# Kernel optimization log

Measured on AMD Instinct MI355X. Metric: run time of the kernel, lower is better.

The kernel has to match this reference:

```python
import jax, jax.numpy as jnp
import numpy as np

DIM = 384
HEADS = 8
ADLA = 343
HWD = 14
N = HWD ** 3
B = 8
HEAD_DIM = DIM // HEADS
SCALE = HEAD_DIM ** -0.5
POOL = 7  # ceil(343**(1/3)); 14 is evenly divisible by 7


def _lin_mat(in_size, out_size):
    # PyTorch trilinear interpolation (align_corners=False), one axis -> (out,in) matrix
    scale = in_size / out_size
    x = (np.arange(out_size) + 0.5) * scale - 0.5
    x = np.clip(x, 0.0, in_size - 1)
    x0 = np.floor(x).astype(np.int64)
    x1 = np.minimum(x0 + 1, in_size - 1)
    w = (x - x0).astype(np.float32)
    M = np.zeros((out_size, in_size), np.float32)
    M[np.arange(out_size), x0] += 1.0 - w
    M[np.arange(out_size), x1] += w
    return jnp.asarray(M)


def _interp3(t, out_hwd):
    # t: (..., a, b, c) -> (..., H, W, D) trilinear, align_corners=False
    Ma = _lin_mat(t.shape[-3], out_hwd[0])
    Mb = _lin_mat(t.shape[-2], out_hwd[1])
    Mc = _lin_mat(t.shape[-1], out_hwd[2])
    return jnp.einsum('...abc,xa,yb,zc->...xyz', t, Ma, Mb, Mc)


def setup_inputs() -> dict:
    key = jax.random.key(0)
    ks = jax.random.split(key, 16)
    std = 0.02
    return {
        'x': jax.random.normal(ks[0], (B, N, DIM), jnp.float32),
        'Wq': jax.random.normal(ks[1], (DIM, DIM), jnp.float32) * std,
        'Wkv': jax.random.normal(ks[2], (DIM, 2 * DIM), jnp.float32) * std,
        'Wproj': jax.random.normal(ks[3], (DIM, DIM), jnp.float32) * std,
        'bproj': jnp.zeros((DIM,), jnp.float32),
        'dwc_w': jax.random.normal(ks[4], (DIM, 1, 3, 3, 3), jnp.float32) * std,
        'dwc_b': jnp.zeros((DIM,), jnp.float32),
        'an_bias': jax.random.normal(ks[5], (HEADS, ADLA, 7, 7, 7), jnp.float32) * std,
        'na_bias': jax.random.normal(ks[6], (HEADS, ADLA, 7, 7, 7), jnp.float32) * std,
        'ah_bias': jax.random.normal(ks[7], (1, HEADS, ADLA, HWD, 1, 1), jnp.float32) * std,
        'aw_bias': jax.random.normal(ks[8], (1, HEADS, ADLA, 1, HWD, 1), jnp.float32) * std,
        'ad_bias': jax.random.normal(ks[9], (1, HEADS, ADLA, 1, 1, HWD), jnp.float32) * std,
        'ha_bias': jax.random.normal(ks[10], (1, HEADS, HWD, 1, 1, ADLA), jnp.float32) * std,
        'wa_bias': jax.random.normal(ks[11], (1, HEADS, 1, HWD, 1, ADLA), jnp.float32) * std,
        'da_bias': jax.random.normal(ks[12], (1, HEADS, 1, 1, HWD, ADLA), jnp.float32) * std,
        'H': HWD, 'W': HWD, 'D': HWD,
    }


def reference(x, Wq, Wkv, Wproj, bproj, dwc_w, dwc_b, an_bias, na_bias,
              ah_bias, aw_bias, ad_bias, ha_bias, wa_bias, da_bias, H, W, D):
    b, n, c = x.shape
    h, hd = HEADS, c // HEADS
    q = x @ Wq                       # (b, n, c)
    kv = x @ Wkv                     # (b, n, 2c)  (sr_ratio == 1)
    k, v = kv[..., :c], kv[..., c:]
    # AdaptiveAvgPool3d 14->7: even 2x2x2 block mean; spatial flatten order matches torch
    adla = q.reshape(b, POOL, H // POOL, POOL, W // POOL, POOL, D // POOL, c)
    adla = adla.mean(axis=(2, 4, 6)).reshape(b, ADLA, c)   # (b, A, c)
    qh = q.reshape(b, n, h, hd).transpose(0, 2, 1, 3)       # (b,h,n,hd)
    kh = k.reshape(b, n, h, hd).transpose(0, 2, 1, 3)
    vh = v.reshape(b, n, h, hd).transpose(0, 2, 1, 3)
    ath = adla.reshape(b, ADLA, h, hd).transpose(0, 2, 1, 3)  # (b,h,A,hd)
    # stage 1: anchor -> tokens
    pb1 = _interp3(an_bias, (H, W, D)).reshape(1, h, ADLA, n)
    pb2 = (ah_bias + aw_bias + ad_bias).reshape(1, h, ADLA, n)
    logits1 = jnp.einsum('bhad,bhnd->bhan', ath * SCALE, kh) + pb1 + pb2
    adla_v = jnp.einsum('bhan,bhnd->bhad', jax.nn.softmax(logits1, axis=-1), vh)
    # stage 2: tokens -> anchor
    ab1 = _interp3(na_bias, (H, W, D)).reshape(1, h, ADLA, n).transpose(0, 1, 3, 2)
    ab2 = (ha_bias + wa_bias + da_bias).reshape(1, h, n, ADLA)
    logits2 = jnp.einsum('bhnd,bhad->bhna', qh * SCALE, ath) + ab1 + ab2
    out = jnp.einsum('bhna,bhad->bhnd', jax.nn.softmax(logits2, axis=-1), adla_v)
    out = out.transpose(0, 2, 1, 3).reshape(b, n, c)
    # depthwise Conv3d on v volume, fused into residual
    vvol = v.reshape(b, H, W, D, c).transpose(0, 4, 1, 2, 3)  # (b,c,H,W,D)
    dwc = jax.lax.conv_general_dilated(
        vvol, dwc_w, (1, 1, 1), 'SAME',
        dimension_numbers=('NCDHW', 'OIDHW', 'NCDHW'), feature_group_count=c)
    dwc = dwc + dwc_b[None, :, None, None, None]
    out = out + dwc.transpose(0, 2, 3, 4, 1).reshape(b, n, c)
    return out @ Wproj + bproj
```

## Files before the change

kernel.cpp:

```cpp
#include <hip/hip_runtime.h>
#include <hip/hip_bf16.h>
#include <cstdint>

typedef __bf16 bf16;
typedef __attribute__((ext_vector_type(8))) __bf16 bf16x8;
typedef __attribute__((ext_vector_type(4))) __bf16 bf16x4;
typedef __attribute__((ext_vector_type(2))) __bf16 bf16x2;
typedef __attribute__((ext_vector_type(4))) float f32x4;

constexpr int DIM = 384;
constexpr int HEAD_DIM = 48;
constexpr int ADLA_N = 343;
constexpr int NTOK = 2744;
constexpr int BATCH = 8;
constexpr int MTOT = BATCH * NTOK;
constexpr float SCALE = 0.14433756729740643f;
constexpr int B1W = 2816;
constexpr int B2W = 384;
constexpr int ADV_W = 352;
constexpr int SEG = 6;

__global__ void transpose_weights(const float* __restrict__ Wq,
                                  const float* __restrict__ Wkv,
                                  const float* __restrict__ Wproj,
                                  bf16* __restrict__ WTall,
                                  bf16* __restrict__ WprojT) {
  int idx = blockIdx.x * 256 + threadIdx.x;
  const int total1 = 1152 * 384;
  if (idx < total1) {
    int j = idx / 384, k = idx % 384;
    WTall[idx] = (bf16)((j < 384) ? Wq[k * 384 + j] : Wkv[k * 768 + (j - 384)]);
  } else {
    int i2 = idx - total1;
    if (i2 < 384 * 384) {
      int j = i2 / 384, k = i2 % 384;
      WprojT[i2] = (bf16)Wproj[k * 384 + j];
    }
  }
}

__device__ __forceinline__ void lin_w(int i, int& i0, int& i1, float& w) {
  float f = 0.5f * (float)i - 0.25f;
  f = fminf(fmaxf(f, 0.0f), 6.0f);
  i0 = (int)f;
  w = f - (float)i0;
  i1 = (i0 + 1 < 7) ? i0 + 1 : 6;
}

__device__ __forceinline__ float interp3(const float* __restrict__ p, int x, int y, int z) {
  int x0, x1, y0, y1, z0, z1; float wx, wy, wz;
  lin_w(x, x0, x1, wx); lin_w(y, y0, y1, wy); lin_w(z, z0, z1, wz);
  float c000 = p[x0*49 + y0*7 + z0], c001 = p[x0*49 + y0*7 + z1];
  float c010 = p[x0*49 + y1*7 + z0], c011 = p[x0*49 + y1*7 + z1];
  float c100 = p[x1*49 + y0*7 + z0], c101 = p[x1*49 + y0*7 + z1];
  float c110 = p[x1*49 + y1*7 + z0], c111 = p[x1*49 + y1*7 + z1];
  float c00 = c000 + wz * (c001 - c000), c01 = c010 + wz * (c011 - c010);
  float c10 = c100 + wz * (c101 - c100), c11 = c110 + wz * (c111 - c110);
  float c0 = c00 + wy * (c01 - c00), c1 = c10 + wy * (c11 - c10);
  return c0 + wx * (c1 - c0);
}

__global__ void bias1_kernel(const float* __restrict__ an, const float* __restrict__ ah,
                             const float* __restrict__ aw, const float* __restrict__ ad,
                             bf16* __restrict__ out) {
  int h = blockIdx.x / ADLA_N, a = blockIdx.x % ADLA_N;
  const float* anp = an + ((size_t)h * ADLA_N + a) * 343;
  const float* ahp = ah + ((size_t)h * ADLA_N + a) * 14;
  const float* awp = aw + ((size_t)h * ADLA_N + a) * 14;
  const float* adp = ad + ((size_t)h * ADLA_N + a) * 14;
  bf16* op = out + ((size_t)h * ADLA_N + a) * B1W;
  for (int n = threadIdx.x; n < B1W; n += 256) {
    if (n < NTOK) {
      int x = n / 196, y = (n / 14) % 14, z = n % 14;
      float v = interp3(anp, x, y, z) + ahp[x] + awp[y] + adp[z];
      op[n] = (bf16)v;
    } else {
      op[n] = (bf16)0.f;
    }
  }
}

__global__ __launch_bounds__(256)
void bias2_kernel(const float* __restrict__ na, const float* __restrict__ ha,
                  const float* __restrict__ wa, const float* __restrict__ da,
                  bf16* __restrict__ out) {
  __shared__ bf16 t[64 * 66];
  const int tid = threadIdx.x;
  const int wv = tid >> 6, lane = tid & 63;
  const int n0 = blockIdx.x * 64, a0 = blockIdx.y * 64;
  const int h = blockIdx.z;
  const int nc = min(n0 + lane, NTOK - 1);
  const int x = nc / 196, y = (nc / 14) % 14, z = nc % 14;
  int x0, x1, y0, y1, z0, z1; float wx, wy, wz;
  lin_w(x, x0, x1, wx); lin_w(y, y0, y1, wy); lin_w(z, z0, z1, wz);
  const int o[8] = { x0*49 + y0*7 + z0, x0*49 + y0*7 + z1,
                     x0*49 + y1*7 + z0, x0*49 + y1*7 + z1,
                     x1*49 + y0*7 + z0, x1*49 + y0*7 + z1,
                     x1*49 + y1*7 + z0, x1*49 + y1*7 + z1 };
  const float wgt[8] = { (1.f-wx)*(1.f-wy)*(1.f-wz), (1.f-wx)*(1.f-wy)*wz,
                         (1.f-wx)*wy*(1.f-wz),       (1.f-wx)*wy*wz,
                         wx*(1.f-wy)*(1.f-wz),       wx*(1.f-wy)*wz,
                         wx*wy*(1.f-wz),             wx*wy*wz };
#pragma unroll
  for (int j = 0; j < 16; j++) {
    const int al = wv * 16 + j;
    const int a = a0 + al;
    float s = 0.f;
    if (a < ADLA_N) {
      const float* p = na + ((size_t)h * ADLA_N + a) * 343;
#pragma unroll
      for (int k = 0; k < 8; k++) s += p[o[k]] * wgt[k];
      s += ha[((size_t)h * 14 + x) * ADLA_N + a]
         + wa[((size_t)h * 14 + y) * ADLA_N + a]
         + da[((size_t)h * 14 + z) * ADLA_N + a];
    }
    t[lane * 66 + al] = (bf16)s;
  }
  __syncthreads();
#pragma unroll
  for (int j = 0; j < 16; j++) {
    const int nr = wv * 16 + j;
    if (n0 + nr < NTOK)
      out[((size_t)h * NTOK + n0 + nr) * B2W + a0 + lane] = t[nr * 66 + lane];
  }
}

template <int MODE, typename AT, typename OT>
__global__ __launch_bounds__(256)
void gemm128(const AT* __restrict__ A, const bf16* __restrict__ BT, int M,
             OT* __restrict__ O0, bf16* __restrict__ O1, bf16* __restrict__ O2,
             const float* __restrict__ bias) {
  __shared__ __align__(16) bf16 As[128 * 40];
  __shared__ __align__(16) bf16 Bs[128 * 40];
  const int tid = threadIdx.x;
  const int wv = tid >> 6, lane = tid & 63;
  const int m0 = blockIdx.x * 128, n0 = blockIdx.y * 128;
  const int wr = wv >> 1, wc = wv & 1;
  f32x4 zero4 = {0.f, 0.f, 0.f, 0.f};
  f32x4 acc[4][4];
#pragma unroll
  for (int i = 0; i < 4; i++)
#pragma unroll
    for (int j = 0; j < 4; j++) acc[i][j] = zero4;

  for (int k0 = 0; k0 < 384; k0 += 32) {
    __syncthreads();
#pragma unroll
    for (int i = 0; i < 2; i++) {
      int flat = i * 256 + tid;
      int row = flat >> 2, cg = flat & 3;
      int gr = m0 + row; if (gr >= M) gr = M - 1;
      bf16x8 av;
      if constexpr (sizeof(AT) == 4) {
        const float4* s4 = (const float4*)(A + (size_t)gr * 384 + k0 + cg * 8);
        float4 a = s4[0], b = s4[1];
        av[0]=(bf16)a.x; av[1]=(bf16)a.y; av[2]=(bf16)a.z; av[3]=(bf16)a.w;
        av[4]=(bf16)b.x; av[5]=(bf16)b.y; av[6]=(bf16)b.z; av[7]=(bf16)b.w;
      } else {
        av = *(const bf16x8*)(A + (size_t)gr * 384 + k0 + cg * 8);
      }
      *(bf16x8*)(As + row * 40 + cg * 8) = av;
      int nr = n0 + row;
      *(bf16x8*)(Bs + row * 40 + cg * 8) = *(const bf16x8*)(BT + (size_t)nr * 384 + k0 + cg * 8);
    }
    __syncthreads();
    bf16x8 af[4], bfr[4];
#pragma unroll
    for (int t = 0; t < 4; t++) {
      af[t]  = *(const bf16x8*)(As + (wr * 64 + t * 16 + (lane & 15)) * 40 + (lane >> 4) * 8);
      bfr[t] = *(const bf16x8*)(Bs + (wc * 64 + t * 16 + (lane & 15)) * 40 + (lane >> 4) * 8);
    }
#pragma unroll
    for (int rt = 0; rt < 4; rt++)
#pragma unroll
      for (int ct = 0; ct < 4; ct++)
        acc[rt][ct] = __builtin_amdgcn_mfma_f32_16x16x32_bf16(af[rt], bfr[ct], acc[rt][ct], 0, 0, 0);
  }
  const int quad = lane >> 4, colL = lane & 15;
#pragma unroll
  for (int rt = 0; rt < 4; rt++) {
#pragma unroll
    for (int ct = 0; ct < 4; ct++) {
      int gcol = n0 + wc * 64 + ct * 16 + colL;
#pragma unroll
      for (int r = 0; r < 4; r++) {
        int grow = m0 + wr * 64 + rt * 16 + quad * 4 + r;
        if (grow < M) {
          float v = acc[rt][ct][r];
          if (MODE == 1) {
            v += bias[gcol];
            O0[(size_t)grow * 384 + gcol] = (OT)v;
          } else {
            bf16* dst; int c;
            if (gcol < 384)      { dst = (bf16*)O0; c = gcol; }
            else if (gcol < 768) { dst = O1; c = gcol - 384; }
            else                 { dst = O2; c = gcol - 768; }
            dst[(size_t)grow * 384 + c] = (bf16)v;
          }
        }
      }
    }
  }
}

__global__ void transpose_v(const bf16* __restrict__ v, bf16* __restrict__ vT) {
  __shared__ bf16 t[64][65];
  int n0 = blockIdx.x * 64, c0 = blockIdx.y * 64, b = blockIdx.z;
  int tid = threadIdx.x;
  int cl = tid & 63, rs = tid >> 6;
  for (int j = 0; j < 16; j++) {
    int r = rs * 16 + j;
    int n = n0 + r;
    if (n < NTOK) t[cl][r] = v[((size_t)b * NTOK + n) * DIM + c0 + cl];
  }
  __syncthreads();
  int nl = tid & 63, cs = tid >> 6;
  int n = n0 + nl;
  if (n < NTOK)
    for (int j = 0; j < 16; j++) {
      int cc = cs * 16 + j;
      vT[((size_t)b * DIM + c0 + cc) * NTOK + n] = t[cc][nl];
    }
}

__global__ void pool_kernel(const bf16* __restrict__ q, bf16* __restrict__ adla) {
  int idx = blockIdx.x * 256 + threadIdx.x;
  if (idx >= BATCH * ADLA_N * DIM) return;
  int c = idx % DIM;
  int a = (idx / DIM) % ADLA_N;
  int b = idx / (DIM * ADLA_N);
  int a0 = a / 49, a1 = (a / 7) % 7, a2 = a % 7;
  float s = 0.f;
#pragma unroll
  for (int i = 0; i < 2; i++)
#pragma unroll
    for (int j = 0; j < 2; j++)
#pragma unroll
      for (int k = 0; k < 2; k++) {
        int n = (a0 * 2 + i) * 196 + (a1 * 2 + j) * 14 + (a2 * 2 + k);
        s += (float)q[((size_t)b * NTOK + n) * DIM + c];
      }
  adla[idx] = (bf16)(s * 0.125f);
}

template <int MODE>
__global__ __launch_bounds__(256, 4)
void attn_kernel(const bf16* __restrict__ Amat, const bf16* __restrict__ Kmat,
                 const bf16* __restrict__ Vt, const bf16* __restrict__ Bias,
                 bf16* __restrict__ Out, float* __restrict__ OutP,
                 float* __restrict__ RsP,
                 int AR, int NC, int biasW,
                 size_t vtB, size_t vtH, int vtS) {
  __shared__ __align__(16) bf16 kT[2][64 * 64];
  __shared__ __align__(16) bf16 vTs[2][48 * 64];
  __shared__ __align__(16) bf16 pT[64 * 64];
  const int tid = threadIdx.x;
  const int wv = tid >> 6, lane = tid & 63;

  int h, bI, rblk, seg;
  {
    const int id = blockIdx.x;
    h = id & 7;
    int t = id >> 3;
    if (MODE == 0) { rblk = t % 6; t /= 6; bI = t & 7; seg = t >> 3; }
    else           { bI = t & 7; rblk = t >> 3; seg = 0; }
  }
  const int bh = bI * 8 + h;
  const int r0 = rblk * 64;
  const int quad = lane >> 4, colL = lane & 15;
  const int rowL = wv * 16 + colL;

  int ar = r0 + rowL; if (ar >= AR) ar = AR - 1;
  const bf16* aRow = Amat + ((size_t)bI * AR + ar) * DIM + h * HEAD_DIM;
  bf16x8 af0 = *(const bf16x8*)(aRow + quad * 8);
  bf16x8 af1;
#pragma unroll
  for (int e = 0; e < 8; e++) af1[e] = (bf16)0.f;
  if (quad < 2) af1 = *(const bf16x8*)(aRow + 32 + quad * 8);

  f32x4 zero4 = {0.f, 0.f, 0.f, 0.f};
  f32x4 acc[3] = {zero4, zero4, zero4};
  float rowsum = 0.f;
  const int nCh = (NC + 63) >> 6;
  const int ch0 = (MODE == 0) ? seg * 8 : 0;
  const int ch1 = (MODE == 0) ? min(nCh, ch0 + 8) : nCh;
  int br = r0 + rowL; if (br >= AR) br = AR - 1;
  const bf16* biasRow = Bias + ((size_t)h * AR + br) * biasW + quad * 4;

  bf16x8 kreg[2], vreg[2];
  auto load_tile = [&](int ch) {
    const int c0 = ch << 6;
#pragma unroll
    for (int i = 0; i < 2; i++) {
      int flat = i * 256 + tid;
      int row = flat >> 3, cg = flat & 7;
      int kg = (cg < 6) ? cg : 0;
      int gr = c0 + row; if (gr >= NC) gr = NC - 1;
      kreg[i] = *(const bf16x8*)(Kmat + ((size_t)bI * NC + gr) * DIM + h * HEAD_DIM + kg * 8);
    }
#pragma unroll
    for (int i = 0; i < 2; i++) {
      int flat = i * 256 + tid;
      int d = flat >> 3; if (d > 47) d = 47;
      int cg = flat & 7;
      int cc = c0 + cg * 8; if (cc > vtS - 8) cc = vtS - 8;
      vreg[i] = *(const bf16x8*)(Vt + (size_t)bI * vtB + (size_t)h * vtH + (size_t)d * vtS + cc);
    }
  };
  auto write_tile = [&](int buf) {
    bf16* kd = kT[buf];
    bf16* vd = vTs[buf];
#pragma unroll
    for (int i = 0; i < 2; i++) {
      int flat = i * 256 + tid;
      int row = flat >> 3, cg = flat & 7;
      *(bf16x8*)(kd + row * 64 + ((cg ^ (row & 7)) << 3)) = kreg[i];
    }
#pragma unroll
    for (int i = 0; i < 2; i++) {
      int flat = i * 256 + tid;
      int d = flat >> 3; if (d > 47) d = 47;
      int cg = flat & 7;
      *(bf16x8*)(vd + d * 64 + ((cg ^ (d & 7)) << 3)) = vreg[i];
    }
  };

  load_tile(ch0);
  write_tile(0);
  __syncthreads();
  int cur = 0;

  for (int ch = ch0; ch < ch1; ch++) {
    const int c0 = ch << 6;
    const bool hasNext = (ch + 1 < ch1);
    if (hasNext) load_tile(ch + 1);

    bf16x4 bv[4];
#pragma unroll
    for (int ct = 0; ct < 4; ct++)
      bv[ct] = *(const bf16x4*)(biasRow + c0 + ct * 16);

    const bf16* kc = kT[cur];
    const bf16* vc = vTs[cur];

    f32x4 sacc[4];
#pragma unroll
    for (int ct = 0; ct < 4; ct++) sacc[ct] = zero4;
#pragma unroll
    for (int ct = 0; ct < 4; ct++) {
      int krow = ct * 16 + colL;
      bf16x8 b0 = *(const bf16x8*)(kc + krow * 64 + ((quad ^ (krow & 7)) << 3));
      bf16x8 b1 = *(const bf16x8*)(kc + krow * 64 + (((4 | quad) ^ (krow & 7)) << 3));
      sacc[ct] = __builtin_amdgcn_mfma_f32_16x16x32_bf16(b0, af0, sacc[ct], 0, 0, 0);
      sacc[ct] = __builtin_amdgcn_mfma_f32_16x16x32_bf16(b1, af1, sacc[ct], 0, 0, 0);
    }
#pragma unroll
    for (int ct = 0; ct < 4; ct++) {
      int cbase = c0 + ct * 16 + quad * 4;
      bf16x4 pw;
#pragma unroll
      for (int j = 0; j < 4; j++) {
        float s = sacc[ct][j] * SCALE + (float)bv[ct][j];
        s = fminf(fmaxf(s, -60.f), 60.f);
        float p = ((cbase + j) < NC) ? __expf(s) : 0.f;
        rowsum += p;
        pw[j] = (bf16)p;
      }
      int g = ct * 2 + (quad >> 1);
      *(bf16x4*)(pT + rowL * 64 + ((g ^ (rowL & 7)) << 3) + (quad & 1) * 4) = pw;
    }
#pragma unroll
    for (int ks = 0; ks < 2; ks++) {
      bf16x8 pf = *(const bf16x8*)(pT + rowL * 64 + (((ks * 4 + quad) ^ (rowL & 7)) << 3));
#pragma unroll
      for (int dt = 0; dt < 3; dt++) {
        const int vrow = dt * 16 + colL;
        bf16x8 vf = *(const bf16x8*)(vc + vrow * 64 + (((ks * 4 + quad) ^ (vrow & 7)) << 3));
        acc[dt] = __builtin_amdgcn_mfma_f32_16x16x32_bf16(pf, vf, acc[dt], 0, 0, 0);
      }
    }
    if (hasNext) write_tile(cur ^ 1);
    __syncthreads();
    cur ^= 1;
  }

  rowsum += __shfl_xor(rowsum, 16, 64);
  rowsum += __shfl_xor(rowsum, 32, 64);

  if (MODE == 0) {
#pragma unroll
    for (int dt = 0; dt < 3; dt++)
#pragma unroll
      for (int r = 0; r < 4; r++) {
        int a = r0 + wv * 16 + quad * 4 + r;
        size_t rowD = ((size_t)seg * 64 + bh) * 48 + dt * 16 + colL;
        if (a < AR)
          OutP[rowD * ADV_W + a] = acc[dt][r];
        else if (a < ADV_W)
          OutP[rowD * ADV_W + a] = 0.f;
      }
    if (quad == 0) {
      int a = r0 + rowL;
      if (a < AR)
        RsP[((size_t)seg * 64 + bh) * ADV_W + a] = rowsum;
    }
  } else {
    float inv[4];
#pragma unroll
    for (int r = 0; r < 4; r++) inv[r] = 1.f / __shfl(rowsum, quad * 4 + r, 64);
#pragma unroll
    for (int dt = 0; dt < 3; dt++)
#pragma unroll
      for (int r = 0; r < 4; r++) {
        int n = r0 + wv * 16 + quad * 4 + r;
        if (n < AR)
          Out[((size_t)bI * AR + n) * DIM + h * HEAD_DIM + dt * 16 + colL] = (bf16)(acc[dt][r] * inv[r]);
      }
  }
}

__global__ void attn1_reduce(const float* __restrict__ advP, const float* __restrict__ rsP,
                             bf16* __restrict__ advT) {
  int idx = blockIdx.x * 256 + threadIdx.x;
  if (idx >= 64 * 48 * ADV_W) return;
  int a = idx % ADV_W;
  int d = (idx / ADV_W) % 48;
  int bh = idx / (ADV_W * 48);
  if (a >= ADLA_N) { advT[idx] = (bf16)0.f; return; }
  float s = 0.f, rs = 0.f;
#pragma unroll
  for (int g = 0; g < SEG; g++) {
    s  += advP[(((size_t)g * 64 + bh) * 48 + d) * ADV_W + a];
    rs += rsP[((size_t)g * 64 + bh) * ADV_W + a];
  }
  advT[((size_t)bh * 48 + d) * ADV_W + a] = (bf16)(s / rs);
}

__global__ __launch_bounds__(256)
void dwc_kernel(const bf16* __restrict__ v, const float* __restrict__ w,
                const float* __restrict__ bias, bf16* __restrict__ io) {
  __shared__ float wts[128 * 27];
  const int tid = threadIdx.x;
  const int cg = blockIdx.y;
  const int b  = blockIdx.z;
  for (int i = tid; i < 128 * 27; i += 256)
    wts[i] = w[(size_t)cg * 128 * 27 + i];
  __syncthreads();

  const int wv = tid >> 6, lane = tid & 63;
  const int xy = blockIdx.x * 4 + wv;
  const int x = xy / 14, y = xy % 14;
  const int c0 = lane * 2;
  const int cglob = cg * 128 + c0;
  const bf16* vb_ = v + (size_t)b * NTOK * DIM + cglob;
  bf16* iob = io + (size_t)b * NTOK * DIM + cglob + (size_t)(x * 196 + y * 14) * DIM;

  float2 acc[14];
#pragma unroll
  for (int z = 0; z < 14; z++) acc[z] = make_float2(0.f, 0.f);

#pragma unroll
  for (int dx = -1; dx <= 1; dx++) {
    int X = x + dx; if ((unsigned)X >= 14u) continue;
#pragma unroll
    for (int dy = -1; dy <= 1; dy++) {
      int Y = y + dy; if ((unsigned)Y >= 14u) continue;
      const bf16* colp = vb_ + (size_t)(X * 196 + Y * 14) * DIM;
      float2 col[14];
#pragma unroll
      for (int z = 0; z < 14; z++) {
        bf16x2 u = *(const bf16x2*)(colp + (size_t)z * DIM);
        col[z] = make_float2((float)u[0], (float)u[1]);
      }
      const int tb = (dx + 1) * 9 + (dy + 1) * 3;
      const float w0a = wts[c0 * 27 + tb],     w0b = wts[(c0 + 1) * 27 + tb];
      const float w1a = wts[c0 * 27 + tb + 1], w1b = wts[(c0 + 1) * 27 + tb + 1];
      const float w2a = wts[c0 * 27 + tb + 2], w2b = wts[(c0 + 1) * 27 + tb + 2];
#pragma unroll
      for (int z = 0; z < 14; z++) {
        float2 s = acc[z];
        if (z > 0)  { s.x += col[z - 1].x * w0a; s.y += col[z - 1].y * w0b; }
        s.x += col[z].x * w1a; s.y += col[z].y * w1b;
        if (z < 13) { s.x += col[z + 1].x * w2a; s.y += col[z + 1].y * w2b; }
        acc[z] = s;
      }
    }
  }

  const float bsa = bias[cglob], bsb = bias[cglob + 1];
#pragma unroll
  for (int z = 0; z < 14; z++) {
    bf16x2 u = *(const bf16x2*)(iob + (size_t)z * DIM);
    bf16x2 o;
    o[0] = (bf16)((float)u[0] + acc[z].x + bsa);
    o[1] = (bf16)((float)u[1] + acc[z].y + bsb);
    *(bf16x2*)(iob + (size_t)z * DIM) = o;
  }
}

extern "C" void kernel_launch(void* const* d_in, const int* in_sizes, int n_in,
                              void* d_out, int out_size, void* d_ws, size_t ws_size,
                              hipStream_t stream) {
  const float* x     = (const float*)d_in[0];
  const float* Wq    = (const float*)d_in[1];
  const float* Wkv   = (const float*)d_in[2];
  const float* Wproj = (const float*)d_in[3];
  const float* bproj = (const float*)d_in[4];
  const float* dwcw  = (const float*)d_in[5];
  const float* dwcb  = (const float*)d_in[6];
  const float* an    = (const float*)d_in[7];
  const float* na    = (const float*)d_in[8];
  const float* ahb   = (const float*)d_in[9];
  const float* awb   = (const float*)d_in[10];
  const float* adb   = (const float*)d_in[11];
  const float* hab   = (const float*)d_in[12];
  const float* wab   = (const float*)d_in[13];
  const float* dab   = (const float*)d_in[14];
  float* out = (float*)d_out;

  uint8_t* ws = (uint8_t*)d_ws;
  size_t off = 0;
  auto carveB = [&](size_t bytes) -> void* {
    void* p = ws + off;
    off += ((bytes + 255) & ~(size_t)255);
    return p;
  };
  auto carve = [&](size_t elems) -> bf16* { return (bf16*)carveB(elems * 2); };
  bf16*  wtall  = carve((size_t)1152 * 384);
  bf16*  wprojT = carve((size_t)384 * 384);
  bf16*  qb     = carve((size_t)MTOT * 384 + 128);
  bf16*  kb     = carve((size_t)MTOT * 384 + 128);
  bf16*  vb     = carve((size_t)MTOT * 384 + 128);
  bf16*  vTb    = carve((size_t)MTOT * 384 + 128);
  bf16*  adla   = carve((size_t)BATCH * ADLA_N * 384 + 128);
  bf16*  advT   = carve((size_t)64 * 48 * ADV_W + 128);
  bf16*  bias1  = carve((size_t)8 * ADLA_N * B1W);
  float* advP   = (float*)carveB((size_t)SEG * 64 * 48 * ADV_W * 4);
  float* rsP    = (float*)carveB((size_t)SEG * 64 * ADV_W * 4);
  bf16*  bias2  = kb;
  bf16*  aout   = vTb;

  transpose_weights<<<dim3((1152 * 384 + 384 * 384 + 255) / 256), 256, 0, stream>>>(
      Wq, Wkv, Wproj, wtall, wprojT);
  bias1_kernel<<<dim3(8 * ADLA_N), 256, 0, stream>>>(an, ahb, awb, adb, bias1);
  gemm128<0, float, bf16><<<dim3(172, 9), 256, 0, stream>>>(
      x, wtall, MTOT, qb, kb, vb, nullptr);
  transpose_v<<<dim3(43, 6, 8), 256, 0, stream>>>(vb, vTb);
  pool_kernel<<<dim3((BATCH * ADLA_N * DIM + 255) / 256), 256, 0, stream>>>(qb, adla);
  attn_kernel<0><<<dim3(6 * 64 * SEG), 256, 0, stream>>>(
      adla, kb, vTb, bias1, nullptr, advP, rsP,
      ADLA_N, NTOK, B1W, (size_t)384 * NTOK, (size_t)48 * NTOK, NTOK);
  attn1_reduce<<<dim3((64 * 48 * ADV_W + 255) / 256), 256, 0, stream>>>(advP, rsP, advT);
  bias2_kernel<<<dim3(43, 6, 8), 256, 0, stream>>>(na, hab, wab, dab, bias2);
  attn_kernel<1><<<dim3(43 * 64), 256, 0, stream>>>(
      qb, adla, advT, bias2, aout, nullptr, nullptr,
      NTOK, ADLA_N, B2W, (size_t)8 * 48 * ADV_W, (size_t)48 * ADV_W, ADV_W);
  dwc_kernel<<<dim3(49, 3, 8), 256, 0, stream>>>(vb, dwcw, dwcb, aout);
  gemm128<1, bf16, float><<<dim3(172, 3), 256, 0, stream>>>(
      aout, wprojT, MTOT, out, nullptr, nullptr, bproj);
}
```

Baseline: 421.9 us.

## Use 512-thread attention blocks over 128 rows and switch softmax to exp2

The attention kernel now runs 8 waves per block covering 128 query/anchor rows, so each K/V tile staged in shared memory serves twice as many rows and each thread loads a single K and V vector per tile. Grid sizes for both attention stages are reduced to match. Separately, both bias tables are pre-multiplied by log2(e) and the scale is folded into a single fma, so the exponential becomes a native exp2 instead of __expf. The trade-offs are larger blocks with more registers and shared memory per block, which may lower occupancy, a clamp range changed to suit exp2, and slightly different bf16 rounding of the biases.

```diff
diff --git a/kernel.cpp b/kernel.cpp
--- a/kernel.cpp
+++ b/kernel.cpp
@@ -15,6 +15,8 @@
 constexpr int BATCH = 8;
 constexpr int MTOT = BATCH * NTOK;
 constexpr float SCALE = 0.14433756729740643f;
+constexpr float LOG2E = 1.4426950408889634f;
+constexpr float SCALE2 = 0.20823512f;
 constexpr int B1W = 2816;
 constexpr int B2W = 384;
 constexpr int ADV_W = 352;
@@ -73,7 +75,7 @@
     if (n < NTOK) {
       int x = n / 196, y = (n / 14) % 14, z = n % 14;
       float v = interp3(anp, x, y, z) + ahp[x] + awp[y] + adp[z];
-      op[n] = (bf16)v;
+      op[n] = (bf16)(v * LOG2E);
     } else {
       op[n] = (bf16)0.f;
     }
@@ -114,7 +116,7 @@
          + wa[((size_t)h * 14 + y) * ADLA_N + a]
          + da[((size_t)h * 14 + z) * ADLA_N + a];
     }
-    t[lane * 66 + al] = (bf16)s;
+    t[lane * 66 + al] = (bf16)(s * LOG2E);
   }
   __syncthreads();
 #pragma unroll
@@ -244,7 +246,7 @@
 }
 
 template <int MODE>
-__global__ __launch_bounds__(256, 4)
+__global__ __launch_bounds__(512, 6)
 void attn_kernel(const bf16* __restrict__ Amat, const bf16* __restrict__ Kmat,
                  const bf16* __restrict__ Vt, const bf16* __restrict__ Bias,
                  bf16* __restrict__ Out, float* __restrict__ OutP,
@@ -253,7 +255,7 @@
                  size_t vtB, size_t vtH, int vtS) {
   __shared__ __align__(16) bf16 kT[2][64 * 64];
   __shared__ __align__(16) bf16 vTs[2][48 * 64];
-  __shared__ __align__(16) bf16 pT[64 * 64];
+  __shared__ __align__(16) bf16 pT[128 * 64];
   const int tid = threadIdx.x;
   const int wv = tid >> 6, lane = tid & 63;
 
@@ -262,11 +264,11 @@
     const int id = blockIdx.x;
     h = id & 7;
     int t = id >> 3;
-    if (MODE == 0) { rblk = t % 6; t /= 6; bI = t & 7; seg = t >> 3; }
+    if (MODE == 0) { rblk = t % 3; t /= 3; bI = t & 7; seg = t >> 3; }
     else           { bI = t & 7; rblk = t >> 3; seg = 0; }
   }
   const int bh = bI * 8 + h;
-  const int r0 = rblk * 64;
+  const int r0 = rblk * 128;
   const int quad = lane >> 4, colL = lane & 15;
   const int rowL = wv * 16 + colL;
 
@@ -287,42 +289,20 @@
   int br = r0 + rowL; if (br >= AR) br = AR - 1;
   const bf16* biasRow = Bias + ((size_t)h * AR + br) * biasW + quad * 4;
 
-  bf16x8 kreg[2], vreg[2];
+  const int srow = tid >> 3, scg = tid & 7;
+  const int skg = (scg < 6) ? scg : 0;
+  const int svd = (srow > 47) ? 47 : srow;
+  bf16x8 kreg, vreg;
   auto load_tile = [&](int ch) {
     const int c0 = ch << 6;
-#pragma unroll
-    for (int i = 0; i < 2; i++) {
-      int flat = i * 256 + tid;
-      int row = flat >> 3, cg = flat & 7;
-      int kg = (cg < 6) ? cg : 0;
-      int gr = c0 + row; if (gr >= NC) gr = NC - 1;
-      kreg[i] = *(const bf16x8*)(Kmat + ((size_t)bI * NC + gr) * DIM + h * HEAD_DIM + kg * 8);
-    }
-#pragma unroll
-    for (int i = 0; i < 2; i++) {
-      int flat = i * 256 + tid;
-      int d = flat >> 3; if (d > 47) d = 47;
-      int cg = flat & 7;
-      int cc = c0 + cg * 8; if (cc > vtS - 8) cc = vtS - 8;
-      vreg[i] = *(const bf16x8*)(Vt + (size_t)bI * vtB + (size_t)h * vtH + (size_t)d * vtS + cc);
-    }
+    int gr = c0 + srow; if (gr >= NC) gr = NC - 1;
+    kreg = *(const bf16x8*)(Kmat + ((size_t)bI * NC + gr) * DIM + h * HEAD_DIM + skg * 8);
+    int cc = c0 + scg * 8; if (cc > vtS - 8) cc = vtS - 8;
+    vreg = *(const bf16x8*)(Vt + (size_t)bI * vtB + (size_t)h * vtH + (size_t)svd * vtS + cc);
   };
   auto write_tile = [&](int buf) {
-    bf16* kd = kT[buf];
-    bf16* vd = vTs[buf];
-#pragma unroll
-    for (int i = 0; i < 2; i++) {
-      int flat = i * 256 + tid;
-      int row = flat >> 3, cg = flat & 7;
-      *(bf16x8*)(kd + row * 64 + ((cg ^ (row & 7)) << 3)) = kreg[i];
-    }
-#pragma unroll
-    for (int i = 0; i < 2; i++) {
-      int flat = i * 256 + tid;
-      int d = flat >> 3; if (d > 47) d = 47;
-      int cg = flat & 7;
-      *(bf16x8*)(vd + d * 64 + ((cg ^ (d & 7)) << 3)) = vreg[i];
-    }
+    *(bf16x8*)(kT[buf] + srow * 64 + ((scg ^ (srow & 7)) << 3)) = kreg;
+    *(bf16x8*)(vTs[buf] + svd * 64 + ((scg ^ (svd & 7)) << 3)) = vreg;
   };
 
   load_tile(ch0);
@@ -360,9 +340,9 @@
       bf16x4 pw;
 #pragma unroll
       for (int j = 0; j < 4; j++) {
-        float s = sacc[ct][j] * SCALE + (float)bv[ct][j];
-        s = fminf(fmaxf(s, -60.f), 60.f);
-        float p = ((cbase + j) < NC) ? __expf(s) : 0.f;
+        float s = fmaf(sacc[ct][j], SCALE2, (float)bv[ct][j]);
+        s = fminf(fmaxf(s, -86.f), 86.f);
+        float p = ((cbase + j) < NC) ? __builtin_amdgcn_exp2f(s) : 0.f;
         rowsum += p;
         pw[j] = (bf16)p;
       }
@@ -547,12 +527,12 @@
       x, wtall, MTOT, qb, kb, vb, nullptr);
   transpose_v<<<dim3(43, 6, 8), 256, 0, stream>>>(vb, vTb);
   pool_kernel<<<dim3((BATCH * ADLA_N * DIM + 255) / 256), 256, 0, stream>>>(qb, adla);
-  attn_kernel<0><<<dim3(6 * 64 * SEG), 256, 0, stream>>>(
+  attn_kernel<0><<<dim3(8 * 3 * 8 * SEG), 512, 0, stream>>>(
       adla, kb, vTb, bias1, nullptr, advP, rsP,
       ADLA_N, NTOK, B1W, (size_t)384 * NTOK, (size_t)48 * NTOK, NTOK);
   attn1_reduce<<<dim3((64 * 48 * ADV_W + 255) / 256), 256, 0, stream>>>(advP, rsP, advT);
   bias2_kernel<<<dim3(43, 6, 8), 256, 0, stream>>>(na, hab, wab, dab, bias2);
-  attn_kernel<1><<<dim3(43 * 64), 256, 0, stream>>>(
+  attn_kernel<1><<<dim3(8 * 8 * 22), 512, 0, stream>>>(
       qb, adla, advT, bias2, aout, nullptr, nullptr,
       NTOK, ADLA_N, B2W, (size_t)8 * 48 * ADV_W, (size_t)48 * ADV_W, ADV_W);
   dwc_kernel<<<dim3(49, 3, 8), 256, 0, stream>>>(vb, dwcw, dwcb, aout);
```

Measured after the change: 429.3 us. About the same (+1.8%).
